# Performance work log

Measured on AMD Instinct MI355X. Metric: run time of the kernel, lower is better.

Reference implementation:

```python
import jax, jax.numpy as jnp
import numpy as np

N_NODES = 50000
N_EDGES = 800000
NODE_DIM = 27
HIDDEN = 64
CTX = 32
HEADS = 4
NEG_SLOPE = 0.2


def _gat_layer(x, src, dst, W, a_src, a_dst, bias, n_nodes):
    # x: [N, F_in], W: [F_in, H*C], a_src/a_dst: [H, C], bias: [C]
    h = (x @ W).reshape(n_nodes, HEADS, -1)            # [N, H, C]
    alpha_src = jnp.einsum('nhc,hc->nh', h, a_src)     # [N, H]
    alpha_dst = jnp.einsum('nhc,hc->nh', h, a_dst)     # [N, H]
    e = alpha_src[src] + alpha_dst[dst]                # [E, H]
    e = jax.nn.leaky_relu(e, NEG_SLOPE)
    # segment softmax over edges grouped by destination node
    e_max = jax.ops.segment_max(e, dst, num_segments=n_nodes)  # [N, H]
    e_exp = jnp.exp(e - e_max[dst])                    # [E, H]
    denom = jax.ops.segment_sum(e_exp, dst, num_segments=n_nodes)  # [N, H]
    alpha = e_exp / denom[dst]                         # [E, H]
    msg = alpha[:, :, None] * h[src]                   # [E, H, C]
    out = jax.ops.segment_sum(msg, dst, num_segments=n_nodes)      # [N, H, C]
    return out.mean(axis=1) + bias                     # concat=False -> head mean


def setup_inputs() -> dict:
    key = jax.random.key(0)
    ks = jax.random.split(key, 16)
    glorot = lambda k, shp: jax.random.normal(k, shp, jnp.float32) * jnp.sqrt(2.0 / (shp[0] + shp[-1]))
    inp = {
        'x': jax.random.normal(ks[0], (N_NODES, NODE_DIM), jnp.float32),
        'edge_index': jax.random.randint(ks[1], (2, N_EDGES), 0, N_NODES, jnp.int32),
        'donor_emb': jax.random.normal(ks[2], (1, CTX), jnp.float32),
        # GAT layer 1
        'W1': glorot(ks[3], (NODE_DIM, HEADS * HIDDEN)),
        'a_src1': glorot(ks[4], (HEADS, HIDDEN)),
        'a_dst1': glorot(ks[5], (HEADS, HIDDEN)),
        'b1': jnp.zeros((HIDDEN,), jnp.float32),
        # GAT layer 2
        'W2': glorot(ks[6], (HIDDEN, HEADS * HIDDEN)),
        'a_src2': glorot(ks[7], (HEADS, HIDDEN)),
        'a_dst2': glorot(ks[8], (HEADS, HIDDEN)),
        'b2': jnp.zeros((HIDDEN,), jnp.float32),
        # scorer MLP
        'Ws1': glorot(ks[9], (HIDDEN + CTX, HIDDEN)),
        'bs1': jnp.zeros((HIDDEN,), jnp.float32),
        'Ws2': glorot(ks[10], (HIDDEN, 1)),
        'bs2': jnp.zeros((1,), jnp.float32),
    }
    return inp


def reference(x, edge_index, donor_emb, W1, a_src1, a_dst1, b1,
              W2, a_src2, a_dst2, b2, Ws1, bs1, Ws2, bs2):
    n = x.shape[0]
    # PyG GATConv default add_self_loops=True
    loop = jnp.arange(n, dtype=edge_index.dtype)
    src = jnp.concatenate([edge_index[0], loop])
    dst = jnp.concatenate([edge_index[1], loop])

    h = jax.nn.elu(_gat_layer(x, src, dst, W1, a_src1, a_dst1, b1, n))
    h = jax.nn.elu(_gat_layer(h, src, dst, W2, a_src2, a_dst2, b2, n))

    ctx = jnp.concatenate([h, jnp.broadcast_to(donor_emb, (n, donor_emb.shape[-1]))], axis=-1)
    hidden = jax.nn.relu(ctx @ Ws1 + bs1)
    logits = (hidden @ Ws2 + bs2).squeeze(-1)          # [N]
    return logits
```

## Files before the change

kernel.cpp:

```cpp
#include <hip/hip_runtime.h>
#include <hip/hip_fp16.h>
#include <cmath>

#define HEADS 4
#define CH 64
#define HC 256
#define NEG 0.2f

typedef __attribute__((ext_vector_type(8))) short short8;
typedef __attribute__((ext_vector_type(4))) float f32x4;
typedef __fp16 half2_t __attribute__((ext_vector_type(2)));

__device__ __forceinline__ float leaky(float v){ return v > 0.f ? v : NEG * v; }

__device__ __forceinline__ short bf16_rne(float f){
    unsigned u = __float_as_uint(f);
    unsigned r = u + 0x7fffu + ((u >> 16) & 1u);
    return (short)(r >> 16);
}
__device__ __forceinline__ float bf16_to_f(short s){
    return __uint_as_float(((unsigned)(unsigned short)s) << 16);
}
__device__ __forceinline__ half2_t bc16(unsigned u){ return __builtin_bit_cast(half2_t, u); }
__device__ __forceinline__ unsigned packh2(float a, float b){
    __half ha = __float2half(a), hb = __float2half(b);
    return (unsigned)__builtin_bit_cast(unsigned short, ha)
         | ((unsigned)__builtin_bit_cast(unsigned short, hb) << 16);
}

__device__ __forceinline__ int block_excl_scan(int v, int* ws4){
    int tid = threadIdx.x, lane = tid & 63, wv = tid >> 6;
    int incl = v;
    #pragma unroll
    for (int off = 1; off < 64; off <<= 1){
        int t = __shfl_up(incl, off);
        if (lane >= off) incl += t;
    }
    if (lane == 63) ws4[wv] = incl;
    __syncthreads();
    int add = 0;
    for (int w = 0; w < wv; ++w) add += ws4[w];
    return incl - v + add;
}


__global__ __launch_bounds__(256) void prep_hist_kernel(
    const float* __restrict__ W1, const float* __restrict__ W2,
    const float* __restrict__ Ws1, const float* __restrict__ bs1,
    const float* __restrict__ donor,
    short* __restrict__ w1hi, short* __restrict__ w2hi,
    short* __restrict__ s1hi, short* __restrict__ s1lo,
    float* __restrict__ d1p,
    const int* __restrict__ ei, int E, int N, int NB, int* __restrict__ bucket_cnt)
{
    if ((int)blockIdx.x < 256){
        int t = blockIdx.x * 256 + threadIdx.x;
        int T = 256 * 256;
        for (int i = t; i < 256 * 40; i += T){
            int n = i / 40, k = i % 40;
            w1hi[i] = bf16_rne((k < 27) ? W1[(size_t)k * HC + n] : 0.f);
        }
        for (int i = t; i < 256 * 72; i += T){
            int n = i / 72, k = i % 72;
            w2hi[i] = bf16_rne((k < 64) ? W2[(size_t)k * HC + n] : 0.f);
        }
        for (int i = t; i < 64 * 72; i += T){
            int n = i / 72, k = i % 72;
            float v = (k < 64) ? Ws1[(size_t)k * 64 + n] : 0.f;
            short hi = bf16_rne(v);
            s1hi[i] = hi; s1lo[i] = bf16_rne(v - bf16_to_f(hi));
        }
        if (t < 64){
            float s = bs1[t];
            for (int k = 0; k < 32; ++k) s = fmaf(donor[k], Ws1[(size_t)(64 + k) * 64 + t], s);
            d1p[t] = s;
        }
    } else {
        __shared__ int lh[256];
        int tid = threadIdx.x;
        int ET = E + N;
        int ebase = ((int)blockIdx.x - 256) * 2048;
        lh[tid] = 0;
        __syncthreads();
        #pragma unroll
        for (int j = 0; j < 8; ++j){
            int e = ebase + j * 256 + tid;
            if (e < ET){
                int d = (e < E) ? ei[E + e] : (e - E);
                atomicAdd(&lh[d >> 8], 1);
            }
        }
        __syncthreads();
        if (tid < NB && lh[tid]) atomicAdd(&bucket_cnt[tid], lh[tid]);
    }
}


__global__ __launch_bounds__(256) void coarse_scatter_kernel(
    const int* __restrict__ ei, int E, int N, int NB,
    const int* __restrict__ bucket_cnt, int* __restrict__ bucket_cursor,
    unsigned* __restrict__ pairs)
{
    __shared__ int ws4[4];
    __shared__ int gbase[256];
    __shared__ int lh[256];
    __shared__ int gb[256];
    int tid = threadIdx.x;
    int ET = E + N;
    {
        int v = (tid < NB) ? bucket_cnt[tid] : 0;
        gbase[tid] = block_excl_scan(v, ws4);
    }
    lh[tid] = 0;
    __syncthreads();
    int ebase = blockIdx.x * 2048;
    int d[8], s[8], r[8];
    #pragma unroll
    for (int j = 0; j < 8; ++j){
        int e = ebase + j * 256 + tid;
        d[j] = -1;
        if (e < ET){
            if (e < E){ s[j] = ei[e]; d[j] = ei[E + e]; } else { s[j] = d[j] = e - E; }
            r[j] = atomicAdd(&lh[d[j] >> 8], 1);
        }
    }
    __syncthreads();
    if (tid < NB && lh[tid]) gb[tid] = gbase[tid] + atomicAdd(&bucket_cursor[tid], lh[tid]);
    __syncthreads();
    #pragma unroll
    for (int j = 0; j < 8; ++j){
        if (d[j] >= 0)
            pairs[gb[d[j] >> 8] + r[j]] = ((unsigned)d[j] << 16) | (unsigned)s[j];
    }
}


__device__ __forceinline__ void fine_sort_body(
    int b, const unsigned* __restrict__ pairs, const int* __restrict__ bucket_cnt, int NB,
    int* __restrict__ colsrc, int* __restrict__ rowptr, int N, int ET)
{
    __shared__ int ws4f[4];
    __shared__ int sb[257];
    __shared__ int hist[256];
    __shared__ int cur[256];
    int tid = threadIdx.x;
    {
        int v = (tid < NB) ? bucket_cnt[tid] : 0;
        int excl = block_excl_scan(v, ws4f);
        sb[tid] = excl;
        if (tid == 255) sb[256] = excl + v;
    }
    hist[tid] = 0;
    __syncthreads();
    int base = sb[b], endb = sb[b + 1];
    int cnt = endb - base;
    int d0 = b << 8;
    for (int i = tid; i < cnt; i += 256){
        unsigned p = pairs[base + i];
        atomicAdd(&hist[(int)(p >> 16) - d0], 1);
    }
    __syncthreads();
    int v = hist[tid];
    int excl = block_excl_scan(v, ws4f);
    cur[tid] = excl;
    if (d0 + tid < N) rowptr[d0 + tid] = base + excl;
    if (b == 0 && tid == 0) rowptr[N] = ET;
    __syncthreads();
    for (int i = tid; i < cnt; i += 256){
        unsigned p = pairs[base + i];
        int r = atomicAdd(&cur[(int)(p >> 16) - d0], 1);
        colsrc[base + r] = (int)(p & 0xFFFFu);
    }
}


template<int FIN, int KSTEPS, int NT, bool X3, bool DIRECT>
__device__ __forceinline__ void transform_body(
    int bx, int by,
    const float* __restrict__ xin, const short* __restrict__ whi, const short* __restrict__ wlo,
    const float* __restrict__ a_src, const float* __restrict__ a_dst,
    __half* __restrict__ h, float* __restrict__ asrc, float* __restrict__ adst, int N)
{
    constexpr int KP = KSTEPS * 32;
    constexpr int XP = KP + 4;
    constexpr int WP = KP + 8;
    constexpr int NCOL = NT * 16;
    __shared__ float xl[DIRECT ? 8 : 64 * XP];
    __shared__ short wt_hi[NCOL * WP];
    __shared__ short wt_lo[X3 ? NCOL * WP : 8];

    const int tid = threadIdx.x;
    const int n0 = bx * 64;
    const int c0 = by * NCOL;

    const int wv = tid >> 6, lane = tid & 63;
    const int quad = lane >> 4, ln = lane & 15;
    const int myrow = wv * 16 + ln;

    float fdir[DIRECT ? KSTEPS * 8 : 1];
    if (DIRECT){
        int n = n0 + myrow;
        #pragma unroll
        for (int ks = 0; ks < KSTEPS; ++ks){
            float4 f0 = make_float4(0.f, 0.f, 0.f, 0.f), f1 = f0;
            if (n < N){
                const float* ap = xin + (size_t)n * FIN + ks * 32 + quad * 8;
                f0 = *(const float4*)ap;
                f1 = *(const float4*)(ap + 4);
            }
            fdir[ks*8+0]=f0.x; fdir[ks*8+1]=f0.y; fdir[ks*8+2]=f0.z; fdir[ks*8+3]=f0.w;
            fdir[ks*8+4]=f1.x; fdir[ks*8+5]=f1.y; fdir[ks*8+6]=f1.z; fdir[ks*8+7]=f1.w;
        }
    } else {
        for (int t = tid; t < 64 * KP; t += 256) {
            int row = t / KP, k = t % KP;
            int n = n0 + row;
            float v = 0.f;
            if (n < N && k < FIN) v = xin[(size_t)n * FIN + k];
            xl[row * XP + k] = v;
        }
    }
    {
        const short8* ghi = (const short8*)(whi + (size_t)c0 * WP);
        short8* lhi = (short8*)wt_hi;
        for (int t = tid; t < NCOL * WP / 8; t += 256) lhi[t] = ghi[t];
        if (X3){
            const short8* glo = (const short8*)(wlo + (size_t)c0 * WP);
            short8* llo = (short8*)wt_lo;
            for (int t = tid; t < NCOL * WP / 8; t += 256) llo[t] = glo[t];
        }
    }
    __syncthreads();

    f32x4 acc[NT];
    #pragma unroll
    for (int i = 0; i < NT; ++i) acc[i] = (f32x4){0.f, 0.f, 0.f, 0.f};

    #pragma unroll
    for (int ks = 0; ks < KSTEPS; ++ks) {
        const int k0 = ks * 32 + quad * 8;
        float fa[8];
        if (DIRECT){
            #pragma unroll
            for (int e = 0; e < 8; ++e) fa[e] = fdir[ks * 8 + e];
        } else {
            const float* ap = xl + myrow * XP + k0;
            float4 f0 = *(const float4*)ap;
            float4 f1 = *(const float4*)(ap + 4);
            fa[0]=f0.x; fa[1]=f0.y; fa[2]=f0.z; fa[3]=f0.w;
            fa[4]=f1.x; fa[5]=f1.y; fa[6]=f1.z; fa[7]=f1.w;
        }
        short8 ahi, alo;
        #pragma unroll
        for (int e = 0; e < 8; ++e) {
            short hi = bf16_rne(fa[e]);
            ahi[e] = hi;
            alo[e] = bf16_rne(fa[e] - bf16_to_f(hi));
        }
        #pragma unroll
        for (int nt = 0; nt < NT; ++nt) {
            short8 bhi = *(const short8*)(wt_hi + (nt * 16 + ln) * WP + k0);
            acc[nt] = __builtin_amdgcn_mfma_f32_16x16x32_bf16(ahi, bhi, acc[nt], 0, 0, 0);
            acc[nt] = __builtin_amdgcn_mfma_f32_16x16x32_bf16(alo, bhi, acc[nt], 0, 0, 0);
            if (X3){
                short8 blo = *(const short8*)(wt_lo + (nt * 16 + ln) * WP + k0);
                acc[nt] = __builtin_amdgcn_mfma_f32_16x16x32_bf16(ahi, blo, acc[nt], 0, 0, 0);
            }
        }
    }

    #pragma unroll
    for (int r = 0; r < 4; ++r) {
        int n = n0 + wv * 16 + quad * 4 + r;
        if (n < N) {
            if (NT == 16) {
                #pragma unroll
                for (int q = 0; q < 4; ++q) {
                    uint2 u;
                    u.x = packh2(acc[q][r],     acc[q + 4][r]);
                    u.y = packh2(acc[q + 8][r], acc[q + 12][r]);
                    *(uint2*)((char*)h + (size_t)n * 512 + (q * 16 + ln) * 8) = u;
                }
            } else {
                #pragma unroll
                for (int q = 0; q < 4; ++q) {
                    unsigned u = packh2(acc[q][r], acc[q + 4][r]);
                    *(unsigned*)((char*)h + (size_t)n * 512 + (q * 16 + ln) * 8 + ((c0 >> 6) << 1)) = u;
                }
            }
        }
    }

    float aS[NT], aD[NT];
    #pragma unroll
    for (int nt = 0; nt < NT; ++nt) {
        aS[nt] = a_src[c0 + nt * 16 + ln];
        aD[nt] = a_dst[c0 + nt * 16 + ln];
    }
    #pragma unroll
    for (int hl = 0; hl < NT / 4; ++hl) {
        #pragma unroll
        for (int r = 0; r < 4; ++r) {
            float ps = 0.f, pd = 0.f;
            #pragma unroll
            for (int i = 0; i < 4; ++i) {
                ps = fmaf(acc[hl * 4 + i][r], aS[hl * 4 + i], ps);
                pd = fmaf(acc[hl * 4 + i][r], aD[hl * 4 + i], pd);
            }
            #pragma unroll
            for (int off = 1; off < 16; off <<= 1) {
                ps += __shfl_xor(ps, off);
                pd += __shfl_xor(pd, off);
            }
            if (ln == 0) {
                int n = n0 + wv * 16 + quad * 4 + r;
                if (n < N) {
                    int hg = c0 / 64 + hl;
                    asrc[n * 4 + hg] = ps;
                    adst[n * 4 + hg] = pd;
                }
            }
        }
    }
}

__global__ __launch_bounds__(256) void transform1_fine_kernel(
    const float* __restrict__ xin, const short* __restrict__ whi,
    const float* __restrict__ a_src, const float* __restrict__ a_dst,
    __half* __restrict__ h, float* __restrict__ asrc, float* __restrict__ adst, int N,
    int nblk, const unsigned* __restrict__ pairs, const int* __restrict__ bucket_cnt, int NB,
    int* __restrict__ colsrc, int* __restrict__ rowptr, int ET)
{
    if ((int)blockIdx.x < nblk) {
        transform_body<27, 1, 16, false, false>(blockIdx.x, 0, xin, whi, nullptr,
                                                a_src, a_dst, h, asrc, adst, N);
    } else {
        fine_sort_body(blockIdx.x - nblk, pairs, bucket_cnt, NB, colsrc, rowptr, N, ET);
    }
}

__global__ __launch_bounds__(256) void transform2_kernel(
    const float* __restrict__ xin, const short* __restrict__ whi,
    const float* __restrict__ a_src, const float* __restrict__ a_dst,
    __half* __restrict__ h, float* __restrict__ asrc, float* __restrict__ adst, int N)
{
    transform_body<64, 2, 16, false, true>(blockIdx.x, 0, xin, whi, nullptr,
                                           a_src, a_dst, h, asrc, adst, N);
}


__global__ __launch_bounds__(256) void aggregate_kernel(
    const int* __restrict__ rowptr, const int* __restrict__ colsrc,
    const __half* __restrict__ h, const float* __restrict__ asrc,
    const float* __restrict__ adst, const float* __restrict__ bias,
    float* __restrict__ hout, int N)
{
    int tid = threadIdx.x;
    int grp = tid >> 5;
    int lane32 = tid & 31;
    int n = blockIdx.x * 8 + grp;
    if (n >= N) return;
    int start = rowptr[n], end = rowptr[n + 1];
    int deg = end - start;
    const float4 ad = *(const float4*)(adst + (size_t)n * 4);

    int src0 = 0;
    float e0 = -1e30f, e1 = -1e30f, e2 = -1e30f, e3 = -1e30f;
    bool v0 = lane32 < deg;
    if (v0){
        src0 = colsrc[start + lane32];
        float4 as = *(const float4*)(asrc + (size_t)src0 * 4);
        e0 = leaky(as.x + ad.x); e1 = leaky(as.y + ad.y);
        e2 = leaky(as.z + ad.z); e3 = leaky(as.w + ad.w);
    }

    float m0, m1, m2, m3, i0, i1, i2, i3, p0, p1, p2, p3;
    if (deg <= 32){
        m0 = e0; m1 = e1; m2 = e2; m3 = e3;
        #pragma unroll
        for (int off = 1; off < 32; off <<= 1){
            m0 = fmaxf(m0, __shfl_xor(m0, off));
            m1 = fmaxf(m1, __shfl_xor(m1, off));
            m2 = fmaxf(m2, __shfl_xor(m2, off));
            m3 = fmaxf(m3, __shfl_xor(m3, off));
        }
        p0 = __expf(e0 - m0);
        p1 = __expf(e1 - m1);
        p2 = __expf(e2 - m2);
        p3 = __expf(e3 - m3);
        float t0 = p0, t1 = p1, t2 = p2, t3 = p3;
        #pragma unroll
        for (int off = 1; off < 32; off <<= 1){
            t0 += __shfl_xor(t0, off);
            t1 += __shfl_xor(t1, off);
            t2 += __shfl_xor(t2, off);
            t3 += __shfl_xor(t3, off);
        }
        i0 = 1.f / t0; i1 = 1.f / t1; i2 = 1.f / t2; i3 = 1.f / t3;
    } else {
        m0 = e0; m1 = e1; m2 = e2; m3 = e3;
        float t0 = v0 ? 1.f : 0.f, t1 = t0, t2 = t0, t3 = t0;
        for (int i = start + 32 + lane32; i < end; i += 32){
            int s = colsrc[i];
            float4 as = *(const float4*)(asrc + (size_t)s * 4);
            float e, nm;
            e = leaky(as.x + ad.x); nm = fmaxf(m0, e); t0 = t0 * __expf(m0 - nm) + __expf(e - nm); m0 = nm;
            e = leaky(as.y + ad.y); nm = fmaxf(m1, e); t1 = t1 * __expf(m1 - nm) + __expf(e - nm); m1 = nm;
            e = leaky(as.z + ad.z); nm = fmaxf(m2, e); t2 = t2 * __expf(m2 - nm) + __expf(e - nm); m2 = nm;
            e = leaky(as.w + ad.w); nm = fmaxf(m3, e); t3 = t3 * __expf(m3 - nm) + __expf(e - nm); m3 = nm;
        }
        #pragma unroll
        for (int off = 1; off < 32; off <<= 1){
            float om, os, nm;
            om = __shfl_xor(m0, off); os = __shfl_xor(t0, off);
            nm = fmaxf(m0, om); t0 = t0 * __expf(m0 - nm) + os * __expf(om - nm); m0 = nm;
            om = __shfl_xor(m1, off); os = __shfl_xor(t1, off);
            nm = fmaxf(m1, om); t1 = t1 * __expf(m1 - nm) + os * __expf(om - nm); m1 = nm;
            om = __shfl_xor(m2, off); os = __shfl_xor(t2, off);
            nm = fmaxf(m2, om); t2 = t2 * __expf(m2 - nm) + os * __expf(om - nm); m2 = nm;
            om = __shfl_xor(m3, off); os = __shfl_xor(t3, off);
            nm = fmaxf(m3, om); t3 = t3 * __expf(m3 - nm) + os * __expf(om - nm); m3 = nm;
        }
        i0 = 1.f / t0; i1 = 1.f / t1; i2 = 1.f / t2; i3 = 1.f / t3;
        p0 = __expf(e0 - m0); p1 = __expf(e1 - m1);
        p2 = __expf(e2 - m2); p3 = __expf(e3 - m3);
    }

    float accA = 0.f, accB = 0.f;
    const int boff = lane32 * 16;
    bool first = true;
    for (int base = start; base < end; base += 32){
        int cnt = end - base; if (cnt > 32) cnt = 32;
        float w0, w1, w2, w3; int off = 0;
        if (first){
            w0 = p0 * i0; w1 = p1 * i1; w2 = p2 * i2; w3 = p3 * i3;
            off = v0 ? src0 * (HC * 2) : 0;
        } else {
            w0 = w1 = w2 = w3 = 0.f;
            if (lane32 < cnt){
                int s = colsrc[base + lane32];
                float4 as = *(const float4*)(asrc + (size_t)s * 4);
                w0 = __expf(leaky(as.x + ad.x) - m0) * i0;
                w1 = __expf(leaky(as.y + ad.y) - m1) * i1;
                w2 = __expf(leaky(as.z + ad.z) - m2) * i2;
                w3 = __expf(leaky(as.w + ad.w) - m3) * i3;
                off = s * (HC * 2);
            }
        }
        first = false;
        half2_t q01 = __builtin_amdgcn_cvt_pkrtz(w0, w1);
        half2_t q23 = __builtin_amdgcn_cvt_pkrtz(w2, w3);
        unsigned wx = __builtin_bit_cast(unsigned, q01);
        unsigned wy = __builtin_bit_cast(unsigned, q23);

        int j = 0;
        for (; j + 2 <= cnt; j += 2){
            int o0 = __shfl(off, j, 32);
            unsigned a0 = __shfl((int)wx, j, 32), b0 = __shfl((int)wy, j, 32);
            int o1 = __shfl(off, j + 1, 32);
            unsigned a1 = __shfl((int)wx, j + 1, 32), b1 = __shfl((int)wy, j + 1, 32);
            uint4 h0 = *(const uint4*)((const char*)h + o0 + boff);
            uint4 h1 = *(const uint4*)((const char*)h + o1 + boff);
            accA = __builtin_amdgcn_fdot2(bc16(h0.x), bc16(a0), accA, false);
            accA = __builtin_amdgcn_fdot2(bc16(h0.y), bc16(b0), accA, false);
            accB = __builtin_amdgcn_fdot2(bc16(h0.z), bc16(a0), accB, false);
            accB = __builtin_amdgcn_fdot2(bc16(h0.w), bc16(b0), accB, false);
            accA = __builtin_amdgcn_fdot2(bc16(h1.x), bc16(a1), accA, false);
            accA = __builtin_amdgcn_fdot2(bc16(h1.y), bc16(b1), accA, false);
            accB = __builtin_amdgcn_fdot2(bc16(h1.z), bc16(a1), accB, false);
            accB = __builtin_amdgcn_fdot2(bc16(h1.w), bc16(b1), accB, false);
        }
        for (; j < cnt; ++j){
            int o0 = __shfl(off, j, 32);
            unsigned a0 = __shfl((int)wx, j, 32), b0 = __shfl((int)wy, j, 32);
            uint4 h0 = *(const uint4*)((const char*)h + o0 + boff);
            accA = __builtin_amdgcn_fdot2(bc16(h0.x), bc16(a0), accA, false);
            accA = __builtin_amdgcn_fdot2(bc16(h0.y), bc16(b0), accA, false);
            accB = __builtin_amdgcn_fdot2(bc16(h0.z), bc16(a0), accB, false);
            accB = __builtin_amdgcn_fdot2(bc16(h0.w), bc16(b0), accB, false);
        }
    }

    float2 bv = *(const float2*)(bias + lane32 * 2);
    float oA = accA * 0.25f + bv.x;
    float oB = accB * 0.25f + bv.y;
    oA = (oA > 0.f) ? oA : expm1f(oA);
    oB = (oB > 0.f) ? oB : expm1f(oB);
    *(float2*)(hout + (size_t)n * CH + lane32 * 2) = make_float2(oA, oB);
}


__global__ __launch_bounds__(256) void scorer_mfma_kernel(
    const float* __restrict__ h2, const short* __restrict__ s1hi, const short* __restrict__ s1lo,
    const float* __restrict__ d1p, const float* __restrict__ Ws2, const float* __restrict__ bs2,
    float* __restrict__ out, int N)
{
    constexpr int WP = 72;
    __shared__ short whi[64 * WP];
    __shared__ short wlo[64 * WP];
    const int tid = threadIdx.x;
    const int n0 = blockIdx.x * 64;

    const int wv = tid >> 6, lane = tid & 63;
    const int quad = lane >> 4, ln = lane & 15;
    const int myrow = wv * 16 + ln;
    const int nme = n0 + myrow;

    float fdir[16];
    #pragma unroll
    for (int ks = 0; ks < 2; ++ks){
        float4 f0 = make_float4(0.f, 0.f, 0.f, 0.f), f1 = f0;
        if (nme < N){
            const float* ap = h2 + (size_t)nme * 64 + ks * 32 + quad * 8;
            f0 = *(const float4*)ap;
            f1 = *(const float4*)(ap + 4);
        }
        fdir[ks*8+0]=f0.x; fdir[ks*8+1]=f0.y; fdir[ks*8+2]=f0.z; fdir[ks*8+3]=f0.w;
        fdir[ks*8+4]=f1.x; fdir[ks*8+5]=f1.y; fdir[ks*8+6]=f1.z; fdir[ks*8+7]=f1.w;
    }
    {
        const short8* ghi = (const short8*)s1hi;
        const short8* glo = (const short8*)s1lo;
        short8* lhi = (short8*)whi;
        short8* llo = (short8*)wlo;
        for (int t = tid; t < 64 * WP / 8; t += 256){ lhi[t] = ghi[t]; llo[t] = glo[t]; }
    }
    __syncthreads();

    f32x4 acc[4];
    #pragma unroll
    for (int i = 0; i < 4; ++i) acc[i] = (f32x4){0.f, 0.f, 0.f, 0.f};

    #pragma unroll
    for (int ks = 0; ks < 2; ++ks) {
        const int k0 = ks * 32 + quad * 8;
        short8 ahi, alo;
        #pragma unroll
        for (int e = 0; e < 8; ++e) {
            float v = fdir[ks * 8 + e];
            short hi = bf16_rne(v);
            ahi[e] = hi;
            alo[e] = bf16_rne(v - bf16_to_f(hi));
        }
        #pragma unroll
        for (int nt = 0; nt < 4; ++nt) {
            short8 bhi = *(const short8*)(whi + (nt * 16 + ln) * WP + k0);
            short8 blo = *(const short8*)(wlo + (nt * 16 + ln) * WP + k0);
            acc[nt] = __builtin_amdgcn_mfma_f32_16x16x32_bf16(ahi, bhi, acc[nt], 0, 0, 0);
            acc[nt] = __builtin_amdgcn_mfma_f32_16x16x32_bf16(alo, bhi, acc[nt], 0, 0, 0);
            acc[nt] = __builtin_amdgcn_mfma_f32_16x16x32_bf16(ahi, blo, acc[nt], 0, 0, 0);
        }
    }

    float d1v[4], w2v[4];
    #pragma unroll
    for (int nt = 0; nt < 4; ++nt){
        d1v[nt] = d1p[nt * 16 + ln];
        w2v[nt] = Ws2[nt * 16 + ln];
    }
    float b2 = bs2[0];
    #pragma unroll
    for (int r = 0; r < 4; ++r){
        float t = 0.f;
        #pragma unroll
        for (int nt = 0; nt < 4; ++nt)
            t = fmaf(fmaxf(acc[nt][r] + d1v[nt], 0.f), w2v[nt], t);
        #pragma unroll
        for (int off = 1; off < 16; off <<= 1) t += __shfl_xor(t, off);
        if (ln == 0){
            int n = n0 + wv * 16 + quad * 4 + r;
            if (n < N) out[n] = t + b2;
        }
    }
}


extern "C" void kernel_launch(void* const* d_in, const int* in_sizes, int n_in,
                              void* d_out, int out_size, void* d_ws, size_t ws_size,
                              hipStream_t stream)
{
    const float* x    = (const float*)d_in[0];
    const int*   ei   = (const int*)  d_in[1];
    const float* donor= (const float*)d_in[2];
    const float* W1   = (const float*)d_in[3];
    const float* as1  = (const float*)d_in[4];
    const float* ad1  = (const float*)d_in[5];
    const float* b1   = (const float*)d_in[6];
    const float* W2   = (const float*)d_in[7];
    const float* as2  = (const float*)d_in[8];
    const float* ad2  = (const float*)d_in[9];
    const float* b2   = (const float*)d_in[10];
    const float* Ws1  = (const float*)d_in[11];
    const float* bs1  = (const float*)d_in[12];
    const float* Ws2  = (const float*)d_in[13];
    const float* bs2  = (const float*)d_in[14];

    const int N  = in_sizes[0] / 27;
    const int E  = in_sizes[1] / 2;
    const int ET = E + N;
    const int NB = (N + 255) / 256;

    char* ws = (char*)d_ws;
    auto alloc = [&](size_t bytes) -> void* {
        void* p = (void*)ws;
        ws += (bytes + 255) / 256 * 256;
        return p;
    };
    int*      rowptr  = (int*)     alloc((size_t)(N + 1) * 4);
    int*      colsrc  = (int*)     alloc((size_t)ET * 4);
    unsigned* pairs   = (unsigned*)alloc((size_t)ET * 4);
    __half*   hbig    = (__half*)  alloc((size_t)N * HC * 2);
    float*    asrc    = (float*)   alloc((size_t)N * 4 * 4);
    float*    adst    = (float*)   alloc((size_t)N * 4 * 4);
    float*    hmid    = (float*)   alloc((size_t)N * CH * 4);
    int*      bucket_cnt    = (int*) alloc(256 * 4);
    int*      bucket_cursor = (int*) alloc(256 * 4);
    short*    w1hi    = (short*)   alloc(256 * 40 * 2);
    short*    w2hi    = (short*)   alloc(256 * 72 * 2);
    short*    s1hi    = (short*)   alloc(64 * 72 * 2);
    short*    s1lo    = (short*)   alloc(64 * 72 * 2);
    float*    d1p     = (float*)   alloc(64 * 4);

    const int nblk = (N + 63) / 64;
    const int hblk = (ET + 2047) / 2048;

    (void)hipMemsetAsync(bucket_cnt, 0, 512 * 4, stream);
    prep_hist_kernel<<<256 + hblk, 256, 0, stream>>>(W1, W2, Ws1, bs1, donor,
        w1hi, w2hi, s1hi, s1lo, d1p, ei, E, N, NB, bucket_cnt);
    coarse_scatter_kernel<<<hblk, 256, 0, stream>>>(ei, E, N, NB, bucket_cnt, bucket_cursor, pairs);
    transform1_fine_kernel<<<nblk + NB, 256, 0, stream>>>(
        x, w1hi, as1, ad1, hbig, asrc, adst, N,
        nblk, pairs, bucket_cnt, NB, colsrc, rowptr, ET);
    aggregate_kernel<<<(N + 7) / 8, 256, 0, stream>>>(
        rowptr, colsrc, hbig, asrc, adst, b1, hmid, N);
    transform2_kernel<<<nblk, 256, 0, stream>>>(
        hmid, w2hi, as2, ad2, hbig, asrc, adst, N);
    aggregate_kernel<<<(N + 7) / 8, 256, 0, stream>>>(
        rowptr, colsrc, hbig, asrc, adst, b2, hmid, N);
    scorer_mfma_kernel<<<nblk, 256, 0, stream>>>(
        hmid, s1hi, s1lo, d1p, Ws2, bs2, (float*)d_out, N);
}
```

Measured before the change: 285.6 us.

## Aggregate raw inputs per head before projection, folding attention vectors into weights

Attention logits are now computed directly from node inputs using precomputed W·a vectors. Each layer gathers the narrow input features (27→32 floats, or 64 halfs) per head instead of the 256-wide projected fp16 features. The weight projection and the 1/HEADS mean are applied afterwards in new post-aggregation MFMA kernels, with the ELU fused there. This reduces gather traffic in the edge-bound aggregation. In exchange it adds a post-aggregate GEMM per layer and an intermediate per-head buffer. It also changes rounding, since layer-2 inputs are stored as fp16 and the aggregated buffer is fp16.

```diff
diff --git a/kernel.cpp b/kernel.cpp
--- a/kernel.cpp
+++ b/kernel.cpp
@@ -2,9 +2,6 @@
 #include <hip/hip_fp16.h>
 #include <cmath>
 
-#define HEADS 4
-#define CH 64
-#define HC 256
 #define NEG 0.2f
 
 typedef __attribute__((ext_vector_type(8))) short short8;
@@ -48,25 +45,32 @@
     const float* __restrict__ W1, const float* __restrict__ W2,
     const float* __restrict__ Ws1, const float* __restrict__ bs1,
     const float* __restrict__ donor,
-    short* __restrict__ w1hi, short* __restrict__ w2hi,
-    short* __restrict__ s1hi, short* __restrict__ s1lo,
-    float* __restrict__ d1p,
+    const float* __restrict__ as1, const float* __restrict__ ad1,
+    const float* __restrict__ as2, const float* __restrict__ ad2,
+    short* __restrict__ w1p, short* __restrict__ w2p,
+    short* __restrict__ s1hi, short* __restrict__ s1lo, float* __restrict__ d1p,
+    float* __restrict__ hat1s, float* __restrict__ hat1d,
+    float* __restrict__ hat2s, float* __restrict__ hat2d,
     const int* __restrict__ ei, int E, int N, int NB, int* __restrict__ bucket_cnt)
 {
     if ((int)blockIdx.x < 256){
         int t = blockIdx.x * 256 + threadIdx.x;
         int T = 256 * 256;
-        for (int i = t; i < 256 * 40; i += T){
-            int n = i / 40, k = i % 40;
-            w1hi[i] = bf16_rne((k < 27) ? W1[(size_t)k * HC + n] : 0.f);
-        }
-        for (int i = t; i < 256 * 72; i += T){
-            int n = i / 72, k = i % 72;
-            w2hi[i] = bf16_rne((k < 64) ? W2[(size_t)k * HC + n] : 0.f);
+        for (int i = t; i < 64 * 136; i += T){
+            int c = i / 136, kk = i % 136; short v = 0;
+            if (kk < 128){ int h = kk >> 5, k = kk & 31;
+                if (k < 27) v = bf16_rne(W1[(size_t)k * 256 + h * 64 + c] * 0.25f); }
+            w1p[i] = v;
+        }
+        for (int i = t; i < 64 * 264; i += T){
+            int c = i / 264, kk = i % 264; short v = 0;
+            if (kk < 256){ int h = kk >> 6, k = kk & 63;
+                v = bf16_rne(W2[(size_t)k * 256 + h * 64 + c] * 0.25f); }
+            w2p[i] = v;
         }
         for (int i = t; i < 64 * 72; i += T){
-            int n = i / 72, k = i % 72;
-            float v = (k < 64) ? Ws1[(size_t)k * 64 + n] : 0.f;
+            int nn = i / 72, k = i % 72;
+            float v = (k < 64) ? Ws1[(size_t)k * 64 + nn] : 0.f;
             short hi = bf16_rne(v);
             s1hi[i] = hi; s1lo[i] = bf16_rne(v - bf16_to_f(hi));
         }
@@ -74,6 +78,27 @@
             float s = bs1[t];
             for (int k = 0; k < 32; ++k) s = fmaf(donor[k], Ws1[(size_t)(64 + k) * 64 + t], s);
             d1p[t] = s;
+        }
+        if (t < 128){
+            int h = t >> 5, k = t & 31;
+            float s = 0.f, d = 0.f;
+            if (k < 27)
+                for (int c = 0; c < 64; ++c){
+                    float w = W1[(size_t)k * 256 + h * 64 + c];
+                    s = fmaf(w, as1[h * 64 + c], s);
+                    d = fmaf(w, ad1[h * 64 + c], d);
+                }
+            hat1s[t] = s; hat1d[t] = d;
+        }
+        if (t < 256){
+            int h = t >> 6, k = t & 63;
+            float s = 0.f, d = 0.f;
+            for (int c = 0; c < 64; ++c){
+                float w = W2[(size_t)k * 256 + h * 64 + c];
+                s = fmaf(w, as2[h * 64 + c], s);
+                d = fmaf(w, ad2[h * 64 + c], d);
+            }
+            hat2s[t] = s; hat2d[t] = d;
         }
     } else {
         __shared__ int lh[256];
@@ -174,186 +199,68 @@
 }
 
 
-template<int FIN, int KSTEPS, int NT, bool X3, bool DIRECT>
-__device__ __forceinline__ void transform_body(
-    int bx, int by,
-    const float* __restrict__ xin, const short* __restrict__ whi, const short* __restrict__ wlo,
-    const float* __restrict__ a_src, const float* __restrict__ a_dst,
-    __half* __restrict__ h, float* __restrict__ asrc, float* __restrict__ adst, int N)
-{
-    constexpr int KP = KSTEPS * 32;
-    constexpr int XP = KP + 4;
-    constexpr int WP = KP + 8;
-    constexpr int NCOL = NT * 16;
-    __shared__ float xl[DIRECT ? 8 : 64 * XP];
-    __shared__ short wt_hi[NCOL * WP];
-    __shared__ short wt_lo[X3 ? NCOL * WP : 8];
-
-    const int tid = threadIdx.x;
-    const int n0 = bx * 64;
-    const int c0 = by * NCOL;
-
-    const int wv = tid >> 6, lane = tid & 63;
-    const int quad = lane >> 4, ln = lane & 15;
-    const int myrow = wv * 16 + ln;
-
-    float fdir[DIRECT ? KSTEPS * 8 : 1];
-    if (DIRECT){
-        int n = n0 + myrow;
-        #pragma unroll
-        for (int ks = 0; ks < KSTEPS; ++ks){
-            float4 f0 = make_float4(0.f, 0.f, 0.f, 0.f), f1 = f0;
-            if (n < N){
-                const float* ap = xin + (size_t)n * FIN + ks * 32 + quad * 8;
-                f0 = *(const float4*)ap;
-                f1 = *(const float4*)(ap + 4);
+__global__ __launch_bounds__(256) void xprep_fine_kernel(
+    const float* __restrict__ x, const float* __restrict__ hat1s, const float* __restrict__ hat1d,
+    float* __restrict__ xp, float* __restrict__ asrc, float* __restrict__ adst, int N,
+    int XB, const unsigned* __restrict__ pairs, const int* __restrict__ bucket_cnt, int NB,
+    int* __restrict__ colsrc, int* __restrict__ rowptr, int ET)
+{
+    if ((int)blockIdx.x < XB){
+        int t0 = blockIdx.x * 256 + threadIdx.x, T = XB * 256;
+        for (int i = t0; i < N * 32; i += T){
+            int nn = i >> 5, k = i & 31;
+            xp[i] = (k < 27) ? x[(size_t)nn * 27 + k] : 0.f;
+        }
+        for (int nn = t0; nn < N; nn += T){
+            float xr[27];
+            #pragma unroll
+            for (int k = 0; k < 27; ++k) xr[k] = x[(size_t)nn * 27 + k];
+            #pragma unroll
+            for (int h = 0; h < 4; ++h){
+                float s = 0.f, d = 0.f;
+                #pragma unroll
+                for (int k = 0; k < 27; ++k){
+                    s = fmaf(xr[k], hat1s[h * 32 + k], s);
+                    d = fmaf(xr[k], hat1d[h * 32 + k], d);
+                }
+                asrc[nn * 4 + h] = s;
+                adst[nn * 4 + h] = d;
             }
-            fdir[ks*8+0]=f0.x; fdir[ks*8+1]=f0.y; fdir[ks*8+2]=f0.z; fdir[ks*8+3]=f0.w;
-            fdir[ks*8+4]=f1.x; fdir[ks*8+5]=f1.y; fdir[ks*8+6]=f1.z; fdir[ks*8+7]=f1.w;
         }
     } else {
-        for (int t = tid; t < 64 * KP; t += 256) {
-            int row = t / KP, k = t % KP;
-            int n = n0 + row;
-            float v = 0.f;
-            if (n < N && k < FIN) v = xin[(size_t)n * FIN + k];
-            xl[row * XP + k] = v;
-        }
-    }
-    {
-        const short8* ghi = (const short8*)(whi + (size_t)c0 * WP);
-        short8* lhi = (short8*)wt_hi;
-        for (int t = tid; t < NCOL * WP / 8; t += 256) lhi[t] = ghi[t];
-        if (X3){
-            const short8* glo = (const short8*)(wlo + (size_t)c0 * WP);
-            short8* llo = (short8*)wt_lo;
-            for (int t = tid; t < NCOL * WP / 8; t += 256) llo[t] = glo[t];
-        }
-    }
-    __syncthreads();
-
-    f32x4 acc[NT];
-    #pragma unroll
-    for (int i = 0; i < NT; ++i) acc[i] = (f32x4){0.f, 0.f, 0.f, 0.f};
-
-    #pragma unroll
-    for (int ks = 0; ks < KSTEPS; ++ks) {
-        const int k0 = ks * 32 + quad * 8;
-        float fa[8];
-        if (DIRECT){
-            #pragma unroll
-            for (int e = 0; e < 8; ++e) fa[e] = fdir[ks * 8 + e];
-        } else {
-            const float* ap = xl + myrow * XP + k0;
-            float4 f0 = *(const float4*)ap;
-            float4 f1 = *(const float4*)(ap + 4);
-            fa[0]=f0.x; fa[1]=f0.y; fa[2]=f0.z; fa[3]=f0.w;
-            fa[4]=f1.x; fa[5]=f1.y; fa[6]=f1.z; fa[7]=f1.w;
-        }
-        short8 ahi, alo;
-        #pragma unroll
-        for (int e = 0; e < 8; ++e) {
-            short hi = bf16_rne(fa[e]);
-            ahi[e] = hi;
-            alo[e] = bf16_rne(fa[e] - bf16_to_f(hi));
-        }
-        #pragma unroll
-        for (int nt = 0; nt < NT; ++nt) {
-            short8 bhi = *(const short8*)(wt_hi + (nt * 16 + ln) * WP + k0);
-            acc[nt] = __builtin_amdgcn_mfma_f32_16x16x32_bf16(ahi, bhi, acc[nt], 0, 0, 0);
-            acc[nt] = __builtin_amdgcn_mfma_f32_16x16x32_bf16(alo, bhi, acc[nt], 0, 0, 0);
-            if (X3){
-                short8 blo = *(const short8*)(wt_lo + (nt * 16 + ln) * WP + k0);
-                acc[nt] = __builtin_amdgcn_mfma_f32_16x16x32_bf16(ahi, blo, acc[nt], 0, 0, 0);
-            }
-        }
-    }
-
-    #pragma unroll
-    for (int r = 0; r < 4; ++r) {
-        int n = n0 + wv * 16 + quad * 4 + r;
-        if (n < N) {
-            if (NT == 16) {
-                #pragma unroll
-                for (int q = 0; q < 4; ++q) {
-                    uint2 u;
-                    u.x = packh2(acc[q][r],     acc[q + 4][r]);
-                    u.y = packh2(acc[q + 8][r], acc[q + 12][r]);
-                    *(uint2*)((char*)h + (size_t)n * 512 + (q * 16 + ln) * 8) = u;
-                }
-            } else {
-                #pragma unroll
-                for (int q = 0; q < 4; ++q) {
-                    unsigned u = packh2(acc[q][r], acc[q + 4][r]);
-                    *(unsigned*)((char*)h + (size_t)n * 512 + (q * 16 + ln) * 8 + ((c0 >> 6) << 1)) = u;
-                }
-            }
-        }
-    }
-
-    float aS[NT], aD[NT];
-    #pragma unroll
-    for (int nt = 0; nt < NT; ++nt) {
-        aS[nt] = a_src[c0 + nt * 16 + ln];
-        aD[nt] = a_dst[c0 + nt * 16 + ln];
-    }
-    #pragma unroll
-    for (int hl = 0; hl < NT / 4; ++hl) {
-        #pragma unroll
-        for (int r = 0; r < 4; ++r) {
-            float ps = 0.f, pd = 0.f;
-            #pragma unroll
-            for (int i = 0; i < 4; ++i) {
-                ps = fmaf(acc[hl * 4 + i][r], aS[hl * 4 + i], ps);
-                pd = fmaf(acc[hl * 4 + i][r], aD[hl * 4 + i], pd);
-            }
-            #pragma unroll
-            for (int off = 1; off < 16; off <<= 1) {
-                ps += __shfl_xor(ps, off);
-                pd += __shfl_xor(pd, off);
-            }
-            if (ln == 0) {
-                int n = n0 + wv * 16 + quad * 4 + r;
-                if (n < N) {
-                    int hg = c0 / 64 + hl;
-                    asrc[n * 4 + hg] = ps;
-                    adst[n * 4 + hg] = pd;
-                }
-            }
-        }
-    }
-}
-
-__global__ __launch_bounds__(256) void transform1_fine_kernel(
-    const float* __restrict__ xin, const short* __restrict__ whi,
-    const float* __restrict__ a_src, const float* __restrict__ a_dst,
-    __half* __restrict__ h, float* __restrict__ asrc, float* __restrict__ adst, int N,
-    int nblk, const unsigned* __restrict__ pairs, const int* __restrict__ bucket_cnt, int NB,
-    int* __restrict__ colsrc, int* __restrict__ rowptr, int ET)
-{
-    if ((int)blockIdx.x < nblk) {
-        transform_body<27, 1, 16, false, false>(blockIdx.x, 0, xin, whi, nullptr,
-                                                a_src, a_dst, h, asrc, adst, N);
+        fine_sort_body(blockIdx.x - XB, pairs, bucket_cnt, NB, colsrc, rowptr, N, ET);
+    }
+}
+
+
+template<int L>
+__device__ __forceinline__ void agg_edge(const char* __restrict__ pay, int boff, int o,
+    unsigned aw, unsigned bw, float* accx, float* accy)
+{
+    half2_t ah = bc16(aw), bh = bc16(bw);
+    float w0 = (float)ah[0], w1 = (float)ah[1], w2 = (float)bh[0], w3 = (float)bh[1];
+    if (L == 1){
+        float xv = *(const float*)(pay + o + boff);
+        accx[0] = fmaf(w0, xv, accx[0]);
+        accx[1] = fmaf(w1, xv, accx[1]);
+        accx[2] = fmaf(w2, xv, accx[2]);
+        accx[3] = fmaf(w3, xv, accx[3]);
     } else {
-        fine_sort_body(blockIdx.x - nblk, pairs, bucket_cnt, NB, colsrc, rowptr, N, ET);
-    }
-}
-
-__global__ __launch_bounds__(256) void transform2_kernel(
-    const float* __restrict__ xin, const short* __restrict__ whi,
-    const float* __restrict__ a_src, const float* __restrict__ a_dst,
-    __half* __restrict__ h, float* __restrict__ asrc, float* __restrict__ adst, int N)
-{
-    transform_body<64, 2, 16, false, true>(blockIdx.x, 0, xin, whi, nullptr,
-                                           a_src, a_dst, h, asrc, adst, N);
-}
-
-
+        unsigned hv = *(const unsigned*)(pay + o + boff);
+        half2_t hh = bc16(hv);
+        float c0 = (float)hh[0], c1 = (float)hh[1];
+        accx[0] = fmaf(w0, c0, accx[0]); accy[0] = fmaf(w0, c1, accy[0]);
+        accx[1] = fmaf(w1, c0, accx[1]); accy[1] = fmaf(w1, c1, accy[1]);
+        accx[2] = fmaf(w2, c0, accx[2]); accy[2] = fmaf(w2, c1, accy[2]);
+        accx[3] = fmaf(w3, c0, accx[3]); accy[3] = fmaf(w3, c1, accy[3]);
+    }
+}
+
+template<int L>
 __global__ __launch_bounds__(256) void aggregate_kernel(
     const int* __restrict__ rowptr, const int* __restrict__ colsrc,
-    const __half* __restrict__ h, const float* __restrict__ asrc,
-    const float* __restrict__ adst, const float* __restrict__ bias,
-    float* __restrict__ hout, int N)
+    const char* __restrict__ pay, const float* __restrict__ asrc,
+    const float* __restrict__ adst, char* __restrict__ gout, int N)
 {
     int tid = threadIdx.x;
     int grp = tid >> 5;
@@ -426,15 +333,16 @@
         p2 = __expf(e2 - m2); p3 = __expf(e3 - m3);
     }
 
-    float accA = 0.f, accB = 0.f;
-    const int boff = lane32 * 16;
+    float accx[4] = {0.f, 0.f, 0.f, 0.f};
+    float accy[4] = {0.f, 0.f, 0.f, 0.f};
+    const int boff = lane32 * 4;
     bool first = true;
     for (int base = start; base < end; base += 32){
         int cnt = end - base; if (cnt > 32) cnt = 32;
         float w0, w1, w2, w3; int off = 0;
         if (first){
             w0 = p0 * i0; w1 = p1 * i1; w2 = p2 * i2; w3 = p3 * i3;
-            off = v0 ? src0 * (HC * 2) : 0;
+            off = v0 ? src0 * 128 : 0;
         } else {
             w0 = w1 = w2 = w3 = 0.f;
             if (lane32 < cnt){
@@ -444,49 +352,207 @@
                 w1 = __expf(leaky(as.y + ad.y) - m1) * i1;
                 w2 = __expf(leaky(as.z + ad.z) - m2) * i2;
                 w3 = __expf(leaky(as.w + ad.w) - m3) * i3;
-                off = s * (HC * 2);
+                off = s * 128;
             }
         }
         first = false;
         half2_t q01 = __builtin_amdgcn_cvt_pkrtz(w0, w1);
         half2_t q23 = __builtin_amdgcn_cvt_pkrtz(w2, w3);
-        unsigned wx = __builtin_bit_cast(unsigned, q01);
-        unsigned wy = __builtin_bit_cast(unsigned, q23);
+        int wx = (int)__builtin_bit_cast(unsigned, q01);
+        int wy = (int)__builtin_bit_cast(unsigned, q23);
 
         int j = 0;
         for (; j + 2 <= cnt; j += 2){
             int o0 = __shfl(off, j, 32);
-            unsigned a0 = __shfl((int)wx, j, 32), b0 = __shfl((int)wy, j, 32);
+            unsigned a0 = (unsigned)__shfl(wx, j, 32), b0 = (unsigned)__shfl(wy, j, 32);
             int o1 = __shfl(off, j + 1, 32);
-            unsigned a1 = __shfl((int)wx, j + 1, 32), b1 = __shfl((int)wy, j + 1, 32);
-            uint4 h0 = *(const uint4*)((const char*)h + o0 + boff);
-            uint4 h1 = *(const uint4*)((const char*)h + o1 + boff);
-            accA = __builtin_amdgcn_fdot2(bc16(h0.x), bc16(a0), accA, false);
-            accA = __builtin_amdgcn_fdot2(bc16(h0.y), bc16(b0), accA, false);
-            accB = __builtin_amdgcn_fdot2(bc16(h0.z), bc16(a0), accB, false);
-            accB = __builtin_amdgcn_fdot2(bc16(h0.w), bc16(b0), accB, false);
-            accA = __builtin_amdgcn_fdot2(bc16(h1.x), bc16(a1), accA, false);
-            accA = __builtin_amdgcn_fdot2(bc16(h1.y), bc16(b1), accA, false);
-            accB = __builtin_amdgcn_fdot2(bc16(h1.z), bc16(a1), accB, false);
-            accB = __builtin_amdgcn_fdot2(bc16(h1.w), bc16(b1), accB, false);
+            unsigned a1 = (unsigned)__shfl(wx, j + 1, 32), b1 = (unsigned)__shfl(wy, j + 1, 32);
+            agg_edge<L>(pay, boff, o0, a0, b0, accx, accy);
+            agg_edge<L>(pay, boff, o1, a1, b1, accx, accy);
         }
         for (; j < cnt; ++j){
             int o0 = __shfl(off, j, 32);
-            unsigned a0 = __shfl((int)wx, j, 32), b0 = __shfl((int)wy, j, 32);
-            uint4 h0 = *(const uint4*)((const char*)h + o0 + boff);
-            accA = __builtin_amdgcn_fdot2(bc16(h0.x), bc16(a0), accA, false);
-            accA = __builtin_amdgcn_fdot2(bc16(h0.y), bc16(b0), accA, false);
-            accB = __builtin_amdgcn_fdot2(bc16(h0.z), bc16(a0), accB, false);
-            accB = __builtin_amdgcn_fdot2(bc16(h0.w), bc16(b0), accB, false);
-        }
-    }
-
-    float2 bv = *(const float2*)(bias + lane32 * 2);
-    float oA = accA * 0.25f + bv.x;
-    float oB = accB * 0.25f + bv.y;
-    oA = (oA > 0.f) ? oA : expm1f(oA);
-    oB = (oB > 0.f) ? oB : expm1f(oB);
-    *(float2*)(hout + (size_t)n * CH + lane32 * 2) = make_float2(oA, oB);
+            unsigned a0 = (unsigned)__shfl(wx, j, 32), b0 = (unsigned)__shfl(wy, j, 32);
+            agg_edge<L>(pay, boff, o0, a0, b0, accx, accy);
+        }
+    }
+
+    if (L == 1){
+        float* g = (float*)gout;
+        #pragma unroll
+        for (int h = 0; h < 4; ++h)
+            g[(size_t)n * 128 + h * 32 + lane32] = accx[h];
+    } else {
+        #pragma unroll
+        for (int h = 0; h < 4; ++h){
+            unsigned u = packh2(accx[h], accy[h]);
+            *(unsigned*)(gout + (size_t)n * 512 + h * 128 + lane32 * 4) = u;
+        }
+    }
+}
+
+
+__global__ __launch_bounds__(256) void t1post_kernel(
+    const float* __restrict__ G1, const short* __restrict__ w1p, const float* __restrict__ b1,
+    const float* __restrict__ hat2s, const float* __restrict__ hat2d,
+    __half* __restrict__ hm16, float* __restrict__ asrc, float* __restrict__ adst, int N)
+{
+    constexpr int WP = 136;
+    __shared__ short wt[64 * WP];
+    const int tid = threadIdx.x;
+    const int n0 = blockIdx.x * 64;
+    const int wv = tid >> 6, lane = tid & 63;
+    const int quad = lane >> 4, ln = lane & 15;
+    const int myrow = wv * 16 + ln;
+    const int nme = n0 + myrow;
+
+    {
+        const short8* g = (const short8*)w1p;
+        short8* l = (short8*)wt;
+        for (int t = tid; t < 64 * WP / 8; t += 256) l[t] = g[t];
+    }
+    __syncthreads();
+
+    f32x4 acc[4];
+    #pragma unroll
+    for (int i = 0; i < 4; ++i) acc[i] = (f32x4){0.f, 0.f, 0.f, 0.f};
+
+    #pragma unroll
+    for (int ks = 0; ks < 4; ++ks){
+        const int k0 = ks * 32 + quad * 8;
+        float4 f0 = make_float4(0.f, 0.f, 0.f, 0.f), f1 = f0;
+        if (nme < N){
+            const float* ap = G1 + (size_t)nme * 128 + k0;
+            f0 = *(const float4*)ap;
+            f1 = *(const float4*)(ap + 4);
+        }
+        float fa[8] = {f0.x, f0.y, f0.z, f0.w, f1.x, f1.y, f1.z, f1.w};
+        short8 ahi, alo;
+        #pragma unroll
+        for (int e = 0; e < 8; ++e){
+            short hi = bf16_rne(fa[e]);
+            ahi[e] = hi;
+            alo[e] = bf16_rne(fa[e] - bf16_to_f(hi));
+        }
+        #pragma unroll
+        for (int nt = 0; nt < 4; ++nt){
+            short8 bhi = *(const short8*)(wt + (nt * 16 + ln) * WP + k0);
+            acc[nt] = __builtin_amdgcn_mfma_f32_16x16x32_bf16(ahi, bhi, acc[nt], 0, 0, 0);
+            acc[nt] = __builtin_amdgcn_mfma_f32_16x16x32_bf16(alo, bhi, acc[nt], 0, 0, 0);
+        }
+    }
+
+    float b1v[4], hs[4][4], hd[4][4];
+    #pragma unroll
+    for (int nt = 0; nt < 4; ++nt) b1v[nt] = b1[nt * 16 + ln];
+    #pragma unroll
+    for (int h = 0; h < 4; ++h)
+        #pragma unroll
+        for (int nt = 0; nt < 4; ++nt){
+            hs[h][nt] = hat2s[h * 64 + nt * 16 + ln];
+            hd[h][nt] = hat2d[h * 64 + nt * 16 + ln];
+        }
+
+    #pragma unroll
+    for (int r = 0; r < 4; ++r){
+        int n = n0 + wv * 16 + quad * 4 + r;
+        float ev[4];
+        #pragma unroll
+        for (int nt = 0; nt < 4; ++nt){
+            float v = acc[nt][r] + b1v[nt];
+            v = (v > 0.f) ? v : expm1f(v);
+            ev[nt] = v;
+        }
+        if (n < N){
+            #pragma unroll
+            for (int nt = 0; nt < 4; ++nt)
+                hm16[(size_t)n * 64 + nt * 16 + ln] = __float2half(ev[nt]);
+        }
+        #pragma unroll
+        for (int h = 0; h < 4; ++h){
+            float ps = 0.f, pd = 0.f;
+            #pragma unroll
+            for (int nt = 0; nt < 4; ++nt){
+                ps = fmaf(ev[nt], hs[h][nt], ps);
+                pd = fmaf(ev[nt], hd[h][nt], pd);
+            }
+            #pragma unroll
+            for (int off = 1; off < 16; off <<= 1){
+                ps += __shfl_xor(ps, off);
+                pd += __shfl_xor(pd, off);
+            }
+            if (ln == 0 && n < N){
+                asrc[n * 4 + h] = ps;
+                adst[n * 4 + h] = pd;
+            }
+        }
+    }
+}
+
+
+__global__ __launch_bounds__(256) void t2post_kernel(
+    const char* __restrict__ G2, const short* __restrict__ w2p, const float* __restrict__ b2,
+    float* __restrict__ hmid2, int N)
+{
+    constexpr int WP = 264;
+    __shared__ short wt[64 * WP];
+    const int tid = threadIdx.x;
+    const int n0 = blockIdx.x * 64;
+    const int wv = tid >> 6, lane = tid & 63;
+    const int quad = lane >> 4, ln = lane & 15;
+    const int myrow = wv * 16 + ln;
+    const int nme = n0 + myrow;
+
+    {
+        const short8* g = (const short8*)w2p;
+        short8* l = (short8*)wt;
+        for (int t = tid; t < 64 * WP / 8; t += 256) l[t] = g[t];
+    }
+    __syncthreads();
+
+    f32x4 acc[4];
+    #pragma unroll
+    for (int i = 0; i < 4; ++i) acc[i] = (f32x4){0.f, 0.f, 0.f, 0.f};
+
+    #pragma unroll
+    for (int ks = 0; ks < 8; ++ks){
+        const int k0 = ks * 32 + quad * 8;
+        uint4 u = make_uint4(0u, 0u, 0u, 0u);
+        if (nme < N)
+            u = *(const uint4*)(G2 + (size_t)nme * 512 + (size_t)k0 * 2);
+        half2_t h0 = bc16(u.x), h1 = bc16(u.y), h2 = bc16(u.z), h3 = bc16(u.w);
+        float fa[8] = {(float)h0[0], (float)h0[1], (float)h1[0], (float)h1[1],
+                       (float)h2[0], (float)h2[1], (float)h3[0], (float)h3[1]};
+        short8 ahi, alo;
+        #pragma unroll
+        for (int e = 0; e < 8; ++e){
+            short hi = bf16_rne(fa[e]);
+            ahi[e] = hi;
+            alo[e] = bf16_rne(fa[e] - bf16_to_f(hi));
+        }
+        #pragma unroll
+        for (int nt = 0; nt < 4; ++nt){
+            short8 bhi = *(const short8*)(wt + (nt * 16 + ln) * WP + k0);
+            acc[nt] = __builtin_amdgcn_mfma_f32_16x16x32_bf16(ahi, bhi, acc[nt], 0, 0, 0);
+            acc[nt] = __builtin_amdgcn_mfma_f32_16x16x32_bf16(alo, bhi, acc[nt], 0, 0, 0);
+        }
+    }
+
+    float b2v[4];
+    #pragma unroll
+    for (int nt = 0; nt < 4; ++nt) b2v[nt] = b2[nt * 16 + ln];
+    #pragma unroll
+    for (int r = 0; r < 4; ++r){
+        int n = n0 + wv * 16 + quad * 4 + r;
+        if (n < N){
+            #pragma unroll
+            for (int nt = 0; nt < 4; ++nt){
+                float v = acc[nt][r] + b2v[nt];
+                v = (v > 0.f) ? v : expm1f(v);
+                hmid2[(size_t)n * 64 + nt * 16 + ln] = v;
+            }
+        }
+    }
 }
 
 
@@ -609,34 +675,45 @@
     int*      rowptr  = (int*)     alloc((size_t)(N + 1) * 4);
     int*      colsrc  = (int*)     alloc((size_t)ET * 4);
     unsigned* pairs   = (unsigned*)alloc((size_t)ET * 4);
-    __half*   hbig    = (__half*)  alloc((size_t)N * HC * 2);
+    float*    xp      = (float*)   alloc((size_t)N * 128);
+    char*     gbuf    = (char*)    alloc((size_t)N * 512);
+    __half*   hm16    = (__half*)  alloc((size_t)N * 128);
+    float*    hmid2   = (float*)   alloc((size_t)N * 256);
     float*    asrc    = (float*)   alloc((size_t)N * 4 * 4);
     float*    adst    = (float*)   alloc((size_t)N * 4 * 4);
-    float*    hmid    = (float*)   alloc((size_t)N * CH * 4);
     int*      bucket_cnt    = (int*) alloc(256 * 4);
     int*      bucket_cursor = (int*) alloc(256 * 4);
-    short*    w1hi    = (short*)   alloc(256 * 40 * 2);
-    short*    w2hi    = (short*)   alloc(256 * 72 * 2);
+    short*    w1p     = (short*)   alloc(64 * 136 * 2);
+    short*    w2p     = (short*)   alloc(64 * 264 * 2);
     short*    s1hi    = (short*)   alloc(64 * 72 * 2);
     short*    s1lo    = (short*)   alloc(64 * 72 * 2);
     float*    d1p     = (float*)   alloc(64 * 4);
+    float*    hat1s   = (float*)   alloc(128 * 4);
+    float*    hat1d   = (float*)   alloc(128 * 4);
+    float*    hat2s   = (float*)   alloc(256 * 4);
+    float*    hat2d   = (float*)   alloc(256 * 4);
 
     const int nblk = (N + 63) / 64;
     const int hblk = (ET + 2047) / 2048;
+    const int XB   = 512;
 
     (void)hipMemsetAsync(bucket_cnt, 0, 512 * 4, stream);
-    prep_hist_kernel<<<256 + hblk, 256, 0, stream>>>(W1, W2, Ws1, bs1, donor,
-        w1hi, w2hi, s1hi, s1lo, d1p, ei, E, N, NB, bucket_cnt);
+    prep_hist_kernel<<<256 + hblk, 256, 0, stream>>>(
+        W1, W2, Ws1, bs1, donor, as1, ad1, as2, ad2,
+        w1p, w2p, s1hi, s1lo, d1p, hat1s, hat1d, hat2s, hat2d,
+        ei, E, N, NB, bucket_cnt);
     coarse_scatter_kernel<<<hblk, 256, 0, stream>>>(ei, E, N, NB, bucket_cnt, bucket_cursor, pairs);
-    transform1_fine_kernel<<<nblk + NB, 256, 0, stream>>>(
-        x, w1hi, as1, ad1, hbig, asrc, adst, N,
-        nblk, pairs, bucket_cnt, NB, colsrc, rowptr, ET);
-    aggregate_kernel<<<(N + 7) / 8, 256, 0, stream>>>(
-        rowptr, colsrc, hbig, asrc, adst, b1, hmid, N);
-    transform2_kernel<<<nblk, 256, 0, stream>>>(
-        hmid, w2hi, as2, ad2, hbig, asrc, adst, N);
-    aggregate_kernel<<<(N + 7) / 8, 256, 0, stream>>>(
-        rowptr, colsrc, hbig, asrc, adst, b2, hmid, N);
+    xprep_fine_kernel<<<XB + NB, 256, 0, stream>>>(
+        x, hat1s, hat1d, xp, asrc, adst, N,
+        XB, pairs, bucket_cnt, NB, colsrc, rowptr, ET);
+    aggregate_kernel<1><<<(N + 7) / 8, 256, 0, stream>>>(
+        rowptr, colsrc, (const char*)xp, asrc, adst, gbuf, N);
+    t1post_kernel<<<nblk, 256, 0, stream>>>(
+        (const float*)gbuf, w1p, b1, hat2s, hat2d, hm16, asrc, adst, N);
+    aggregate_kernel<2><<<(N + 7) / 8, 256, 0, stream>>>(
+        rowptr, colsrc, (const char*)hm16, asrc, adst, gbuf, N);
+    t2post_kernel<<<nblk, 256, 0, stream>>>(
+        (const char*)gbuf, w2p, b2, hmid2, N);
     scorer_mfma_kernel<<<nblk, 256, 0, stream>>>(
-        hmid, s1hi, s1lo, d1p, Ws2, bs2, (float*)d_out, N);
-}
+        hmid2, s1hi, s1lo, d1p, Ws2, bs2, (float*)d_out, N);
+}
```

New measurement: 233.3 us. 18.3% less time.
